# Optimization experiments

Hardware: AMD Instinct MI355X
Metric: run time of the kernel (lower is better)

## Reference

```python
import jax, jax.numpy as jnp
import numpy as np

B, C, H, W = 16, 256, 128, 128
HIDE = C // 2  # in_channel // ratio


def setup_inputs() -> dict:
    key = jax.random.key(0)
    k0, k1, k2, k3, k4 = jax.random.split(key, 5)
    x = jax.random.normal(k0, (B, C, H, W), dtype=jnp.float32)
    # conv1: Conv2d(C, HIDE, 1, bias=False) -> weight (HIDE, C)
    w1 = jax.random.normal(k1, (HIDE, C), dtype=jnp.float32) * 0.05
    # conv2/conv3: Conv1d(1, 1, 1, bias=False) -> single scalar each
    w2 = jax.random.normal(k2, (), dtype=jnp.float32)
    w3 = jax.random.normal(k3, (), dtype=jnp.float32)
    # conv4: Conv2d(HIDE, C, 1, bias=False) -> weight (C, HIDE)
    w4 = jax.random.normal(k4, (C, HIDE), dtype=jnp.float32) * 0.05
    # A2 parameter initialized to 1e-6 (as in the torch module)
    A2 = jnp.full((HIDE, HIDE), 1e-6, dtype=jnp.float32)
    return {"x": x, "w1": w1, "w2": w2, "w3": w3, "w4": w4, "A2": A2}


def reference(x, w1, w2, w3, w4, A2):
    # Global average pool: (B, C, H, W) -> (B, C)
    y = jnp.mean(x, axis=(2, 3))
    # conv1 (1x1): (B, C) -> (B, HIDE)
    y = y @ w1.T
    # conv2 (Conv1d 1->1, k=1) is a scalar multiply; softmax over channel dim
    s = jax.nn.softmax(w2 * y, axis=-1)  # (B, HIDE)
    # A1 = s expanded to (B, HIDE, HIDE) with identical rows; A = eye*A1 + A2
    # => y @ A = y * s + y @ A2 (avoids materializing (B,HIDE,HIDE))
    y = y * s + y @ A2
    # conv3 (scalar) + relu
    y = jax.nn.relu(w3 * y)
    # conv4 (1x1): (B, HIDE) -> (B, C), then sigmoid gate
    gate = jax.nn.sigmoid(y @ w4.T)  # (B, C)
    # Broadcast channel gate over the full feature map
    return x * gate[:, :, None, None]
```

## Files before the change

kernel.cpp:

```cpp
#include <hip/hip_runtime.h>
#include <math.h>

#define Bn   16
#define Cn   256
#define Hn   128
#define Wn   128
#define HIDE 128
#define HW   (Hn * Wn)

typedef __attribute__((ext_vector_type(4))) float f32x4;

__global__ __launch_bounds__(256) void mean_kernel(const float* __restrict__ x,
                                                   float* __restrict__ y) {
    const int bc  = blockIdx.x;
    const int tid = threadIdx.x;
    const f32x4* xp = (const f32x4*)(x + (size_t)bc * HW);

    float sum = 0.f;
#pragma unroll
    for (int k = 0; k < HW / 4 / 256; ++k) {
        f32x4 v = xp[tid + k * 256];
        sum += (v.x + v.y) + (v.z + v.w);
    }
    for (int off = 32; off > 0; off >>= 1)
        sum += __shfl_down(sum, off, 64);

    __shared__ float ls[4];
    if ((tid & 63) == 0) ls[tid >> 6] = sum;
    __syncthreads();
    if (tid == 0) {
        float s = (ls[0] + ls[1]) + (ls[2] + ls[3]);
        y[bc] = s * (1.0f / (float)HW);
    }
}

__global__ __launch_bounds__(256) void gate_kernel(const float* __restrict__ y,
                                                   const float* __restrict__ w1,
                                                   const float* __restrict__ w2s,
                                                   const float* __restrict__ w3s,
                                                   const float* __restrict__ w4,
                                                   const float* __restrict__ A2,
                                                   float* __restrict__ gate) {
    const int b   = blockIdx.x;
    const int tid = threadIdx.x;

    __shared__ float sy[Cn];
    __shared__ float sh[HIDE];
    __shared__ float st[HIDE];
    __shared__ float red[2];

    sy[tid] = y[b * Cn + tid];
    __syncthreads();

    const float w2 = w2s[0];
    const float w3 = w3s[0];

    if (tid < HIDE) {
        float acc = 0.f;
        const float* wr = w1 + tid * Cn;
#pragma unroll 4
        for (int c = 0; c < Cn; ++c) acc = fmaf(sy[c], wr[c], acc);
        sh[tid] = acc;
    }
    __syncthreads();

    if (tid == 0) {
        float m = -1e30f;
        for (int j = 0; j < HIDE; ++j) m = fmaxf(m, w2 * sh[j]);
        float s = 0.f;
        for (int j = 0; j < HIDE; ++j) s += expf(w2 * sh[j] - m);
        red[0] = m;
        red[1] = s;
    }
    __syncthreads();
    const float m = red[0], denom = red[1];

    if (tid < HIDE) {
        float sj  = expf(w2 * sh[tid] - m) / denom;
        float acc = sh[tid] * sj;
        for (int k = 0; k < HIDE; ++k) acc = fmaf(sh[k], A2[k * HIDE + tid], acc);
        float t = w3 * acc;
        st[tid] = t > 0.f ? t : 0.f;
    }
    __syncthreads();

    {
        float acc = 0.f;
        const float* wr = w4 + tid * HIDE;
#pragma unroll 4
        for (int j = 0; j < HIDE; ++j) acc = fmaf(st[j], wr[j], acc);
        gate[b * Cn + tid] = 1.f / (1.f + expf(-acc));
    }
}

__global__ __launch_bounds__(256) void scale_kernel(const float* __restrict__ x,
                                                    const float* __restrict__ gate,
                                                    float* __restrict__ out) {
    const int bc  = blockIdx.x;
    const int tid = threadIdx.x;
    const float g = gate[bc];
    const f32x4* xp = (const f32x4*)(x   + (size_t)bc * HW);
    f32x4*       op = (f32x4*)      (out + (size_t)bc * HW);

#pragma unroll
    for (int k = 0; k < HW / 4 / 256; ++k) {
        f32x4 v = xp[tid + k * 256];
        v *= g;
        __builtin_nontemporal_store(v, &op[tid + k * 256]);
    }
}

extern "C" void kernel_launch(void* const* d_in, const int* in_sizes, int n_in,
                              void* d_out, int out_size, void* d_ws, size_t ws_size,
                              hipStream_t stream) {
    const float* x  = (const float*)d_in[0];
    const float* w1 = (const float*)d_in[1];
    const float* w2 = (const float*)d_in[2];
    const float* w3 = (const float*)d_in[3];
    const float* w4 = (const float*)d_in[4];
    const float* A2 = (const float*)d_in[5];
    float* out = (float*)d_out;

    float* y    = (float*)d_ws;
    float* gate = y + Bn * Cn;

    mean_kernel <<<Bn * Cn, 256, 0, stream>>>(x, y);
    gate_kernel <<<Bn,      256, 0, stream>>>(y, w1, w2, w3, w4, A2, gate);
    scale_kernel<<<Bn * Cn, 256, 0, stream>>>(x, gate, out);
}
```

Before: 509.5 us.

## Fuse mean and gate kernels via last-block atomic counter per batch

Merges the global-average-pool kernel with the gate MLP kernel: each block atomically increments a per-batch counter, and the last block to finish for a batch computes that batch's gate. This removes one kernel launch and lets gate computation overlap with remaining pooling blocks. The softmax max/sum reductions are also parallelised with wavefront shuffles instead of a single-thread loop. It adds a memset launch and atomic/fence overhead.

```diff
diff --git a/kernel.cpp b/kernel.cpp
--- a/kernel.cpp
+++ b/kernel.cpp
@@ -10,45 +10,48 @@
 
 typedef __attribute__((ext_vector_type(4))) float f32x4;
 
-__global__ __launch_bounds__(256) void mean_kernel(const float* __restrict__ x,
-                                                   float* __restrict__ y) {
+__global__ __launch_bounds__(256) void mean_gate_kernel(
+    const float* __restrict__ x,
+    const float* __restrict__ w1,
+    const float* __restrict__ w2s,
+    const float* __restrict__ w3s,
+    const float* __restrict__ w4,
+    const float* __restrict__ A2,
+    float* __restrict__ y,
+    float* __restrict__ gate,
+    unsigned int* __restrict__ counters)
+{
     const int bc  = blockIdx.x;
+    const int b   = bc >> 8;
     const int tid = threadIdx.x;
+
+    __shared__ float ls[4];
+    __shared__ int   isLast;
+    __shared__ float sy[Cn];
+    __shared__ float sh[HIDE];
+    __shared__ float st[HIDE];
+    __shared__ float red[4];
+
     const f32x4* xp = (const f32x4*)(x + (size_t)bc * HW);
-
     float sum = 0.f;
 #pragma unroll
-    for (int k = 0; k < HW / 4 / 256; ++k) {
-        f32x4 v = xp[tid + k * 256];
+    for (int i = 0; i < HW / 4 / 256; ++i) {
+        f32x4 v = xp[tid + i * 256];
         sum += (v.x + v.y) + (v.z + v.w);
     }
-    for (int off = 32; off > 0; off >>= 1)
-        sum += __shfl_down(sum, off, 64);
-
-    __shared__ float ls[4];
+    for (int off = 32; off; off >>= 1) sum += __shfl_down(sum, off, 64);
     if ((tid & 63) == 0) ls[tid >> 6] = sum;
     __syncthreads();
     if (tid == 0) {
-        float s = (ls[0] + ls[1]) + (ls[2] + ls[3]);
-        y[bc] = s * (1.0f / (float)HW);
+        y[bc] = ((ls[0] + ls[1]) + (ls[2] + ls[3])) * (1.0f / (float)HW);
+        __threadfence();
+        unsigned old = atomicAdd(&counters[b], 1u);
+        isLast = (old == Cn - 1);
     }
-}
+    __syncthreads();
+    if (!isLast) return;
 
-__global__ __launch_bounds__(256) void gate_kernel(const float* __restrict__ y,
-                                                   const float* __restrict__ w1,
-                                                   const float* __restrict__ w2s,
-                                                   const float* __restrict__ w3s,
-                                                   const float* __restrict__ w4,
-                                                   const float* __restrict__ A2,
-                                                   float* __restrict__ gate) {
-    const int b   = blockIdx.x;
-    const int tid = threadIdx.x;
-
-    __shared__ float sy[Cn];
-    __shared__ float sh[HIDE];
-    __shared__ float st[HIDE];
-    __shared__ float red[2];
-
+    __threadfence();
     sy[tid] = y[b * Cn + tid];
     __syncthreads();
 
@@ -64,21 +67,30 @@
     }
     __syncthreads();
 
-    if (tid == 0) {
-        float m = -1e30f;
-        for (int j = 0; j < HIDE; ++j) m = fmaxf(m, w2 * sh[j]);
-        float s = 0.f;
-        for (int j = 0; j < HIDE; ++j) s += expf(w2 * sh[j] - m);
-        red[0] = m;
-        red[1] = s;
+    if (tid < HIDE) {
+        float v = w2 * sh[tid];
+        for (int off = 32; off; off >>= 1)
+            v = fmaxf(v, __shfl_xor(v, off, 64));
+        if ((tid & 63) == 0) red[tid >> 6] = v;
     }
     __syncthreads();
-    const float m = red[0], denom = red[1];
+    const float m = fmaxf(red[0], red[1]);
+
+    float e = 0.f;
+    if (tid < HIDE) {
+        e = expf(w2 * sh[tid] - m);
+        float s = e;
+        for (int off = 32; off; off >>= 1) s += __shfl_xor(s, off, 64);
+        if ((tid & 63) == 0) red[2 + (tid >> 6)] = s;
+    }
+    __syncthreads();
+    const float denom = red[2] + red[3];
 
     if (tid < HIDE) {
-        float sj  = expf(w2 * sh[tid] - m) / denom;
+        float sj  = e / denom;
         float acc = sh[tid] * sj;
-        for (int k = 0; k < HIDE; ++k) acc = fmaf(sh[k], A2[k * HIDE + tid], acc);
+        for (int kk = 0; kk < HIDE; ++kk)
+            acc = fmaf(sh[kk], A2[kk * HIDE + tid], acc);
         float t = w3 * acc;
         st[tid] = t > 0.f ? t : 0.f;
     }
@@ -103,10 +115,10 @@
     f32x4*       op = (f32x4*)      (out + (size_t)bc * HW);
 
 #pragma unroll
-    for (int k = 0; k < HW / 4 / 256; ++k) {
-        f32x4 v = xp[tid + k * 256];
+    for (int i = 0; i < HW / 4 / 256; ++i) {
+        f32x4 v = xp[tid + i * 256];
         v *= g;
-        __builtin_nontemporal_store(v, &op[tid + k * 256]);
+        __builtin_nontemporal_store(v, &op[tid + i * 256]);
     }
 }
 
@@ -121,10 +133,13 @@
     const float* A2 = (const float*)d_in[5];
     float* out = (float*)d_out;
 
-    float* y    = (float*)d_ws;
-    float* gate = y + Bn * Cn;
+    float*        y        = (float*)d_ws;
+    float*        gate     = y + Bn * Cn;
+    unsigned int* counters = (unsigned int*)(gate + Bn * Cn);
 
-    mean_kernel <<<Bn * Cn, 256, 0, stream>>>(x, y);
-    gate_kernel <<<Bn,      256, 0, stream>>>(y, w1, w2, w3, w4, A2, gate);
-    scale_kernel<<<Bn * Cn, 256, 0, stream>>>(x, gate, out);
+    hipMemsetAsync(counters, 0, Bn * sizeof(unsigned int), stream);
+
+    mean_gate_kernel<<<Bn * Cn, 256, 0, stream>>>(x, w1, w2, w3, w4, A2,
+                                                  y, gate, counters);
+    scale_kernel   <<<Bn * Cn, 256, 0, stream>>>(x, gate, out);
 }
```

Result: slower. 752.4 us (+47.7%).
